# Performance work log

Hardware: AMD Instinct MI355X
Metric: run time of the kernel (lower is better)

The kernel has to match this reference:

```python
import jax, jax.numpy as jnp
import numpy as np

N_NODES = 20000
N_EDGES = 600000
HID = 128
HEADS = 4
NUM_IN = 2 * HID
N_BATCH = 64


def _gelu(x):
    return jax.nn.gelu(x, approximate=False)


def _bn(x, g, b, eps=1e-5):
    # BatchNorm1d, training-mode math: biased variance over the batch dim
    m = jnp.mean(x, axis=0)
    v = jnp.var(x, axis=0)
    return g * (x - m) * jax.lax.rsqrt(v + eps) + b


def setup_inputs() -> dict:
    keys = iter(jax.random.split(jax.random.key(0), 64))

    def nk():
        return next(keys)

    def lin(i, o):
        return (jax.random.normal(nk(), (i, o), jnp.float32) / np.sqrt(i)).astype(jnp.float32)

    def zeros(o):
        return jnp.zeros((o,), jnp.float32)

    inp = {
        "h_V": jax.random.normal(nk(), (N_NODES, HID), jnp.float32),
        "h_E": jax.random.normal(nk(), (N_EDGES, HID), jnp.float32),
        "edge_idx": jax.random.randint(nk(), (2, N_EDGES), 0, N_NODES),
        "batch_id": jnp.sort(jax.random.randint(nk(), (N_NODES,), 0, N_BATCH)),
        # NeighborAttention.W_V (num_in -> hid -> hid -> hid)
        "wv1_w": lin(NUM_IN, HID), "wv1_b": zeros(HID),
        "wv2_w": lin(HID, HID), "wv2_b": zeros(HID),
        "wv3_w": lin(HID, HID), "wv3_b": zeros(HID),
        # NeighborAttention.Bias (3*hid -> hid -> hid -> heads)
        "bb1_w": lin(3 * HID, HID), "bb1_b": zeros(HID),
        "bb2_w": lin(HID, HID), "bb2_b": zeros(HID),
        "bb3_w": lin(HID, HEADS), "bb3_b": zeros(HEADS),
        # NeighborAttention.W_O (no bias)
        "wo_w": lin(HID, HID),
        # GeneralGNN norms 0 and 1
        "n0_g": jnp.ones((HID,), jnp.float32), "n0_b": zeros(HID),
        "n1_g": jnp.ones((HID,), jnp.float32), "n1_b": zeros(HID),
        # dense FFN (hid -> 4*hid -> hid)
        "d1_w": lin(HID, 4 * HID), "d1_b": zeros(4 * HID),
        "d2_w": lin(4 * HID, HID), "d2_b": zeros(HID),
        # EdgeMLP (3*hid -> hid -> hid -> hid) + its norm
        "e1_w": lin(3 * HID, HID), "e1_b": zeros(HID),
        "e2_w": lin(HID, HID), "e2_b": zeros(HID),
        "e3_w": lin(HID, HID), "e3_b": zeros(HID),
        "en_g": jnp.ones((HID,), jnp.float32), "en_b": zeros(HID),
    }
    return inp


def _forward(h_V, h_E, src, dst,
             wv1_w, wv1_b, wv2_w, wv2_b, wv3_w, wv3_b,
             bb1_w, bb1_b, bb2_w, bb2_b, bb3_w, bb3_b,
             wo_w, n0_g, n0_b, n1_g, n1_b,
             d1_w, d1_b, d2_w, d2_b,
             e1_w, e1_b, e2_w, e2_b, e3_w, e3_b, en_g, en_b):
    N = h_V.shape[0]
    d_head = HID // HEADS
    # attention input: cat([h_E, h_V[dst]]) with center_id = src
    h_E_in = jnp.concatenate([h_E, h_V[dst]], axis=-1)  # (E, 2*HID)
    x = jnp.concatenate([h_V[src], h_E_in], axis=-1)     # (E, 3*HID)
    # Bias MLP -> per-edge per-head logits; the sqrt(d) * 1/sqrt(d) scaling cancels
    w = _gelu(x @ bb1_w + bb1_b)
    w = _gelu(w @ bb2_w + bb2_b)
    w = w @ bb3_w + bb3_b                                 # (E, HEADS)
    # value MLP
    V = _gelu(h_E_in @ wv1_w + wv1_b)
    V = _gelu(V @ wv2_w + wv2_b)
    V = (V @ wv3_w + wv3_b).reshape(-1, HEADS, d_head)    # (E, HEADS, d)
    # scatter_softmax over edges sharing a source node
    m = jax.ops.segment_max(w, src, num_segments=N)
    m = jnp.where(jnp.isfinite(m), m, 0.0)
    ew = jnp.exp(w - m[src])
    denom = jax.ops.segment_sum(ew, src, num_segments=N)
    attend = ew / denom[src]                              # (E, HEADS)
    agg = jax.ops.segment_sum(attend[:, :, None] * V, src, num_segments=N)
    dh = agg.reshape(N, HID) @ wo_w                       # W_O
    h_V = _bn(h_V + dh, n0_g, n0_b)
    dh = _gelu(h_V @ d1_w + d1_b) @ d2_w + d2_b           # dense FFN
    h_V = _bn(h_V + dh, n1_g, n1_b)
    # EdgeMLP update
    h_EV = jnp.concatenate([h_V[src], h_E, h_V[dst]], axis=-1)
    msg = _gelu(h_EV @ e1_w + e1_b)
    msg = _gelu(msg @ e2_w + e2_b)
    msg = msg @ e3_w + e3_b
    h_E = _bn(h_E + msg, en_g, en_b)
    # Context with node_context=edge_context=0 is identity
    return (h_V, h_E)


def reference(h_V, h_E, edge_idx, batch_id,
              wv1_w, wv1_b, wv2_w, wv2_b, wv3_w, wv3_b,
              bb1_w, bb1_b, bb2_w, bb2_b, bb3_w, bb3_b,
              wo_w, n0_g, n0_b, n1_g, n1_b,
              d1_w, d1_b, d2_w, d2_b,
              e1_w, e1_b, e2_w, e2_b, e3_w, e3_b, en_g, en_b):
    src, dst = edge_idx[0], edge_idx[1]
    return _forward(h_V, h_E, src, dst,
                    wv1_w, wv1_b, wv2_w, wv2_b, wv3_w, wv3_b,
                    bb1_w, bb1_b, bb2_w, bb2_b, bb3_w, bb3_b,
                    wo_w, n0_g, n0_b, n1_g, n1_b,
                    d1_w, d1_b, d2_w, d2_b,
                    e1_w, e1_b, e2_w, e2_b, e3_w, e3_b, en_g, en_b)
```

## Files before the change

### kernel.cpp

```cpp
#include <hip/hip_runtime.h>
#include <cstdint>
#include <cstddef>

#define NN 20000
#define NE 600000

typedef unsigned short u16;
typedef unsigned int   u32;
typedef __bf16 bf16x8 __attribute__((ext_vector_type(8)));
typedef float  f32x4  __attribute__((ext_vector_type(4)));

constexpr int PK_BB1 = 0;
constexpr int PK_BB2 = PK_BB1 + 384 * 128;
constexpr int PK_WV1 = PK_BB2 + 128 * 128;
constexpr int PK_WV2 = PK_WV1 + 256 * 128;
constexpr int PK_WV3 = PK_WV2 + 128 * 128;
constexpr int PK_WO  = PK_WV3 + 128 * 128;
constexpr int PK_D1  = PK_WO  + 128 * 128;
constexpr int PK_D2  = PK_D1  + 128 * 512;
constexpr int PK_E1  = PK_D2  + 512 * 128;
constexpr int PK_E2  = PK_E1  + 384 * 128;
constexpr int PK_E3  = PK_E2  + 128 * 128;
constexpr int PK_BB3 = PK_E3  + 128 * 128;

constexpr size_t WS_PW    = 0;
constexpr size_t WS_STATS = 0x100000;
constexpr size_t WS_FLAG  = WS_STATS + 3072;
constexpr size_t WS_HIST  = WS_STATS + 0x1000;
constexpr size_t WS_OFFS  = WS_HIST + 0x14000;
constexpr size_t WS_CNT   = WS_OFFS + 0x14000;
constexpr size_t WS_EIDS  = WS_CNT + 0x14000;
constexpr size_t WS_WLOG  = WS_EIDS + 0x250000;
constexpr size_t WS_AGG   = WS_WLOG + 0x930000;
constexpr size_t WS_R     = WS_AGG + 0xA00000;

__device__ __forceinline__ float bf2f(u16 u) {
    return __builtin_bit_cast(float, (u32)u << 16);
}
__device__ __forceinline__ u16 f2bf(float f) {
    return __builtin_bit_cast(u16, static_cast<__bf16>(f));
}
__device__ __forceinline__ float gelu_f(float x) {
    float z = fabsf(x) * 0.70710678118654752f;
    float t = __builtin_amdgcn_rcpf(fmaf(0.3275911f, z, 1.0f));
    float p = t * fmaf(t, fmaf(t, fmaf(t, fmaf(t, 1.061405429f, -1.453152027f),
                                       1.421413741f), -0.284496736f), 0.254829592f);
    float erfz = fmaf(-p, __expf(-z * z), 1.0f);
    float u = 0.5f * x;
    return fmaf(copysignf(erfz, x), u, u);
}
__device__ __forceinline__ float ldv(const void* p, size_t i, int m) {
    return m ? ((const float*)p)[i] : bf2f(((const u16*)p)[i]);
}
#define MFMA(a, b, c) __builtin_amdgcn_mfma_f32_16x16x32_bf16(a, b, c, 0, 0, 0)

#define TM 32
#define XS 136

__device__ __forceinline__ void mma128(const u16* __restrict__ xl, const u16* __restrict__ wp,
                                       int kcBase, int nDiv16, int wave, int lane,
                                       f32x4 acc[2][2]) {
#pragma unroll
    for (int kc = 0; kc < 4; ++kc) {
        int koff = kc * 32 + (lane >> 4) * 8;
        bf16x8 a0 = *(const bf16x8*)&xl[((lane & 15)) * XS + koff];
        bf16x8 a1 = *(const bf16x8*)&xl[((lane & 15) + 16) * XS + koff];
#pragma unroll
        for (int ni = 0; ni < 2; ++ni) {
            int nc = wave * 2 + ni;
            bf16x8 b = *(const bf16x8*)&wp[(((size_t)(kcBase + kc) * nDiv16 + nc) * 64 + lane) * 8];
            acc[0][ni] = MFMA(a0, b, acc[0][ni]);
            acc[1][ni] = MFMA(a1, b, acc[1][ni]);
        }
    }
}

__device__ __forceinline__ void epi_lds(f32x4 acc[2][2], u16* hl, const void* biasG,
                                        int wave, int lane, bool doGelu, int f32m) {
    int col0 = wave * 32;
#pragma unroll
    for (int ni = 0; ni < 2; ++ni) {
        int col = col0 + ni * 16 + (lane & 15);
        float b = ldv(biasG, col, f32m);
#pragma unroll
        for (int mi = 0; mi < 2; ++mi) {
            int rb = mi * 16 + (lane >> 4) * 4;
#pragma unroll
            for (int r = 0; r < 4; ++r) {
                float v = acc[mi][ni][r] + b;
                if (doGelu) v = gelu_f(v);
                hl[(rb + r) * XS + col] = f2bf(v);
            }
        }
    }
}

__device__ __forceinline__ void stage_row8(u16* dst8, const void* table, size_t row, int c8, int f32m) {
    if (f32m) {
        const float* s = (const float*)table + row * 128 + c8 * 8;
        float4 v0 = *(const float4*)s;
        float4 v1 = *(const float4*)(s + 4);
        uint4 o;
        o.x = (u32)f2bf(v0.x) | ((u32)f2bf(v0.y) << 16);
        o.y = (u32)f2bf(v0.z) | ((u32)f2bf(v0.w) << 16);
        o.z = (u32)f2bf(v1.x) | ((u32)f2bf(v1.y) << 16);
        o.w = (u32)f2bf(v1.z) | ((u32)f2bf(v1.w) << 16);
        *(uint4*)dst8 = o;
    } else {
        *(uint4*)dst8 = *(const uint4*)((const u16*)table + row * 128 + c8 * 8);
    }
}

__device__ __forceinline__ void stage_gidx(u16* dst, const void* table, const int* gIdx,
                                           int tid, int f32m) {
    int r0 = tid >> 4, c = tid & 15;
#pragma unroll
    for (int p = 0; p < 2; ++p) {
        int r = r0 + p * 16;
        stage_row8(&dst[r * XS + c * 8], table, (size_t)gIdx[r], c, f32m);
    }
}
__device__ __forceinline__ void stage_seq(u16* dst, const void* table, size_t rowBase, int tid, int f32m) {
    int r0 = tid >> 4, c = tid & 15;
#pragma unroll
    for (int p = 0; p < 2; ++p) {
        int r = r0 + p * 16;
        stage_row8(&dst[r * XS + c * 8], table, rowBase + r, c, f32m);
    }
}

__global__ void k_detect(const void* hV, int* flag) {
    int l = threadIdx.x;
    const u16* p = (const u16*)hV;
    float m = fmaxf(fabsf(bf2f(p[l])), fabsf(bf2f(p[64 + l])));
    for (int s = 1; s < 64; s <<= 1) m = fmaxf(m, __shfl_xor(m, s));
    if (l == 0) *flag = (m > 1e4f) ? 1 : 0;
}

__global__ void k_pack(const void* bb1, const void* bb2, const void* wv1, const void* wv2,
                       const void* wv3, const void* wo, const void* d1, const void* d2,
                       const void* e1, const void* e2, const void* e3, const void* bb3,
                       u16* pw, const int* dflag) {
    int f32m = *dflag;
    const int Ks[12] = {384, 128, 256, 128, 128, 128, 128, 512, 384, 128, 128, 128};
    const int Ns[12] = {128, 128, 128, 128, 128, 128, 512, 128, 128, 128, 128, 16};
    const void* srcs[12] = {bb1, bb2, wv1, wv2, wv3, wo, d1, d2, e1, e2, e3, bb3};
    int gid = blockIdx.x * 256 + threadIdx.x;
    int lane = gid & 63;
    int fid = gid >> 6;
    if (fid >= 708) return;
    int w = 0, base = 0, dstoff = 0;
    for (int i = 0; i < 12; ++i) {
        int nf = (Ks[i] / 32) * (Ns[i] / 16);
        if (fid < base + nf) { w = i; break; }
        base += nf;
        dstoff += Ks[i] * Ns[i];
    }
    int f = fid - base;
    int N = Ns[w];
    int kc = f / (N / 16), nc = f % (N / 16);
    const void* S = srcs[w];
    u16* D = pw + dstoff + ((size_t)f * 64 + lane) * 8;
    int krow = kc * 32 + (lane >> 4) * 8;
    int col = nc * 16 + (lane & 15);
#pragma unroll
    for (int j = 0; j < 8; ++j) {
        float v;
        if (w == 11) v = (col < 4) ? ldv(S, (size_t)(krow + j) * 4 + col, f32m) : 0.f;
        else         v = ldv(S, (size_t)(krow + j) * N + col, f32m);
        D[j] = f2bf(v);
    }
}

__global__ void k_hist(const int* src, int* hist) {
    int e = blockIdx.x * 256 + threadIdx.x;
    if (e < NE) atomicAdd(&hist[src[e]], 1);
}

__global__ void k_scan(const int* hist, int* offs, int* cnt) {
    __shared__ int buf[1024];
    __shared__ int carry;
    if (threadIdx.x == 0) carry = 0;
    __syncthreads();
    for (int b = 0; b < NN; b += 1024) {
        int i = b + threadIdx.x;
        int v = (i < NN) ? hist[i] : 0;
        buf[threadIdx.x] = v;
        __syncthreads();
        for (int s = 1; s < 1024; s <<= 1) {
            int t = (threadIdx.x >= s) ? buf[threadIdx.x - s] : 0;
            __syncthreads();
            buf[threadIdx.x] += t;
            __syncthreads();
        }
        int excl = buf[threadIdx.x] - v + carry;
        if (i < NN) { offs[i] = excl; cnt[i] = excl; }
        __syncthreads();
        if (threadIdx.x == 1023) carry += buf[1023];
        __syncthreads();
    }
    if (threadIdx.x == 0) offs[NN] = carry;
}

__global__ void k_fill(const int* src, int* cnt, int* eids) {
    int e = blockIdx.x * 256 + threadIdx.x;
    if (e < NE) {
        int slot = atomicAdd(&cnt[src[e]], 1);
        eids[slot] = e;
    }
}

__global__ __launch_bounds__(256, 2) void k_edge1(
    const void* __restrict__ hV, const void* __restrict__ hE, const int* __restrict__ eidx,
    const u16* __restrict__ pw, const void* bb1b, const void* bb2b,
    const void* bb3b, const void* wv1b, const void* wv2b, const void* wv3b,
    float* __restrict__ wlog, void* __restrict__ dout, const int* dflag) {
    __shared__ __attribute__((aligned(16))) u16 X[TM * XS];
    __shared__ __attribute__((aligned(16))) u16 Y[TM * XS];
    __shared__ __attribute__((aligned(16))) u16 Z[TM * XS];
    int f32m = *dflag;
    int tid = threadIdx.x, wave = tid >> 6, lane = tid & 63;
    long e0 = (long)blockIdx.x * TM;

    stage_gidx(X, hV, eidx + e0, tid, f32m);
    stage_seq (Y, hE, (size_t)e0, tid, f32m);
    stage_gidx(Z, hV, eidx + NE + e0, tid, f32m);
    __syncthreads();
    f32x4 accB[2][2] = {};
    f32x4 accV[2][2] = {};
    mma128(X, pw + PK_BB1, 0, 8, wave, lane, accB);
    mma128(Y, pw + PK_BB1, 4, 8, wave, lane, accB);
    mma128(Z, pw + PK_BB1, 8, 8, wave, lane, accB);
    mma128(Y, pw + PK_WV1, 0, 8, wave, lane, accV);
    mma128(Z, pw + PK_WV1, 4, 8, wave, lane, accV);
    __syncthreads();
    epi_lds(accB, X, bb1b, wave, lane, true, f32m);
    epi_lds(accV, Y, wv1b, wave, lane, true, f32m);
    __syncthreads();
    f32x4 accB2[2][2] = {};
    f32x4 accV2[2][2] = {};
    mma128(X, pw + PK_BB2, 0, 8, wave, lane, accB2);
    mma128(Y, pw + PK_WV2, 0, 8, wave, lane, accV2);
    __syncthreads();
    epi_lds(accB2, Z, bb2b, wave, lane, true, f32m);
    epi_lds(accV2, X, wv2b, wave, lane, true, f32m);
    __syncthreads();
    u16* Vout = (u16*)((char*)dout + (size_t)NN * 128 * (f32m ? 4 : 2));
    f32x4 accV3[2][2] = {};
    mma128(X, pw + PK_WV3, 0, 8, wave, lane, accV3);
    {
        int col0 = wave * 32;
#pragma unroll
        for (int ni = 0; ni < 2; ++ni) {
            int col = col0 + ni * 16 + (lane & 15);
            float b = ldv(wv3b, col, f32m);
#pragma unroll
            for (int mi = 0; mi < 2; ++mi) {
                int rb = mi * 16 + (lane >> 4) * 4;
#pragma unroll
                for (int r = 0; r < 4; ++r) {
                    long row = e0 + rb + r;
                    Vout[row * 128 + col] = f2bf(accV3[mi][ni][r] + b);
                }
            }
        }
    }
    if (wave == 0) {
        f32x4 aw0 = {0.f, 0.f, 0.f, 0.f};
        f32x4 aw1 = {0.f, 0.f, 0.f, 0.f};
#pragma unroll
        for (int kc = 0; kc < 4; ++kc) {
            int koff = kc * 32 + (lane >> 4) * 8;
            bf16x8 a0 = *(const bf16x8*)&Z[(lane & 15) * XS + koff];
            bf16x8 a1 = *(const bf16x8*)&Z[((lane & 15) + 16) * XS + koff];
            bf16x8 b = *(const bf16x8*)&pw[PK_BB3 + ((size_t)kc * 64 + lane) * 8];
            aw0 = MFMA(a0, b, aw0);
            aw1 = MFMA(a1, b, aw1);
        }
        if ((lane & 15) < 4) {
            int col = lane & 15;
            int rbase = (lane >> 4) * 4;
            float b3 = ldv(bb3b, col, f32m);
#pragma unroll
            for (int r = 0; r < 4; ++r) {
                wlog[(e0 + rbase + r) * 4 + col] = aw0[r] + b3;
                wlog[(e0 + 16 + rbase + r) * 4 + col] = aw1[r] + b3;
            }
        }
    }
}

__global__ void k_agg(const int* __restrict__ offs, const int* __restrict__ eids,
                      const float* __restrict__ wlog, const void* __restrict__ dout,
                      float* __restrict__ agg, const int* dflag) {
    int f32m = *dflag;
    const u16* V = (const u16*)((const char*)dout + (size_t)NN * 128 * (f32m ? 4 : 2));
    int node = blockIdx.x;
    int l = threadIdx.x;
    int beg = offs[node], end = offs[node + 1];
    int deg = end - beg;
    if (deg == 0) {
        agg[(size_t)node * 128 + 2 * l] = 0.f;
        agg[(size_t)node * 128 + 2 * l + 1] = 0.f;
        return;
    }
    int h = l & 3;
    float lmax = -3.0e38f;
    for (int i = (l >> 2); i < deg; i += 16) {
        int e = eids[beg + i];
        lmax = fmaxf(lmax, wlog[(size_t)e * 4 + h]);
    }
    for (int s = 4; s < 64; s <<= 1) lmax = fmaxf(lmax, __shfl_xor(lmax, s));
    float lsum = 0.f;
    for (int i = (l >> 2); i < deg; i += 16) {
        int e = eids[beg + i];
        lsum += __expf(wlog[(size_t)e * 4 + h] - lmax);
    }
    for (int s = 4; s < 64; s <<= 1) lsum += __shfl_xor(lsum, s);
    int hh = l >> 4;
    float mh = __shfl(lmax, hh);
    float inv = __builtin_amdgcn_rcpf(__shfl(lsum, hh));
    float a0 = 0.f, a1 = 0.f;
    for (int i = 0; i < deg; ++i) {
        int e = eids[beg + i];
        float aw = __expf(wlog[(size_t)e * 4 + hh] - mh) * inv;
        u32 vv = *(const u32*)&V[(size_t)e * 128 + 2 * l];
        a0 += aw * bf2f((u16)(vv & 0xffffu));
        a1 += aw * bf2f((u16)(vv >> 16));
    }
    float2 o;
    o.x = a0;
    o.y = a1;
    *(float2*)&agg[(size_t)node * 128 + 2 * l] = o;
}

__global__ __launch_bounds__(256, 2) void k_wo(const float* __restrict__ agg,
                                               const void* __restrict__ hV,
                                               const u16* __restrict__ pw,
                                               float* __restrict__ rbuf,
                                               float* __restrict__ stats0, const int* dflag) {
    __shared__ __attribute__((aligned(16))) u16 xb[TM * XS];
    __shared__ float lsum[128], lsq[128];
    int f32m = *dflag;
    int tid = threadIdx.x, wave = tid >> 6, lane = tid & 63;
    long n0 = (long)blockIdx.x * TM;
    if (tid < 128) { lsum[tid] = 0.f; lsq[tid] = 0.f; }
    {
        int r = tid >> 3, cc = (tid & 7) * 16;
        long row = n0 + r;
        for (int j = 0; j < 16; j += 4) {
            float4 v = {0.f, 0.f, 0.f, 0.f};
            if (row < NN) v = *(const float4*)&agg[row * 128 + cc + j];
            u16* d = &xb[r * XS + cc + j];
            d[0] = f2bf(v.x); d[1] = f2bf(v.y); d[2] = f2bf(v.z); d[3] = f2bf(v.w);
        }
    }
    __syncthreads();
    f32x4 acc[2][2] = {};
    mma128(xb, pw + PK_WO, 0, 8, wave, lane, acc);
    int col0 = wave * 32;
#pragma unroll
    for (int ni = 0; ni < 2; ++ni) {
        int col = col0 + ni * 16 + (lane & 15);
#pragma unroll
        for (int mi = 0; mi < 2; ++mi) {
            int rb = mi * 16 + (lane >> 4) * 4;
#pragma unroll
            for (int r = 0; r < 4; ++r) {
                long row = n0 + rb + r;
                if (row < NN) {
                    float v = ldv(hV, (size_t)row * 128 + col, f32m) + acc[mi][ni][r];
                    rbuf[row * 128 + col] = v;
                    atomicAdd(&lsum[col], v);
                    atomicAdd(&lsq[col], v * v);
                }
            }
        }
    }
    __syncthreads();
    if (tid < 128) {
        atomicAdd(&stats0[tid], lsum[tid]);
        atomicAdd(&stats0[128 + tid], lsq[tid]);
    }
}

__global__ __launch_bounds__(256, 2) void k_ffn(float* __restrict__ rbuf,
                                                const float* __restrict__ stats0,
                                                const void* n0g, const void* n0b,
                                                const u16* __restrict__ pw,
                                                const void* d1b, const void* d2b,
                                                float* __restrict__ stats1, const int* dflag) {
    __shared__ float bnS[128], bnB[128];
    __shared__ float h1f[TM * 128];
    __shared__ __attribute__((aligned(16))) u16 h1x[TM * XS];
    __shared__ __attribute__((aligned(16))) u16 hid[TM * 520];
    __shared__ float lsum[128], lsq[128];
    int f32m = *dflag;
    int tid = threadIdx.x, wave = tid >> 6, lane = tid & 63;
    long n0 = (long)blockIdx.x * TM;
    if (tid < 128) {
        float m = stats0[tid] * (1.f / NN);
        float v = stats0[128 + tid] * (1.f / NN) - m * m;
        float s = ldv(n0g, tid, f32m) * rsqrtf(v + 1e-5f);
        bnS[tid] = s;
        bnB[tid] = ldv(n0b, tid, f32m) - m * s;
        lsum[tid] = 0.f;
        lsq[tid] = 0.f;
    }
    __syncthreads();
    {
        int r = tid >> 3, cc = (tid & 7) * 16;
        long row = n0 + r;
        for (int j = 0; j < 16; ++j) {
            int c = cc + j;
            float v = (row < NN) ? (rbuf[row * 128 + c] * bnS[c] + bnB[c]) : 0.f;
            h1f[r * 128 + c] = v;
            h1x[r * XS + c] = f2bf(v);
        }
    }
    __syncthreads();
    f32x4 acc1[2][8] = {};
#pragma unroll
    for (int kc = 0; kc < 4; ++kc) {
        int koff = kc * 32 + (lane >> 4) * 8;
        bf16x8 a0 = *(const bf16x8*)&h1x[(lane & 15) * XS + koff];
        bf16x8 a1 = *(const bf16x8*)&h1x[((lane & 15) + 16) * XS + koff];
#pragma unroll
        for (int ni = 0; ni < 8; ++ni) {
            int nc = wave * 8 + ni;
            bf16x8 b = *(const bf16x8*)&pw[PK_D1 + (((size_t)kc * 32 + nc) * 64 + lane) * 8];
            acc1[0][ni] = MFMA(a0, b, acc1[0][ni]);
            acc1[1][ni] = MFMA(a1, b, acc1[1][ni]);
        }
    }
#pragma unroll
    for (int ni = 0; ni < 8; ++ni) {
        int col = wave * 128 + ni * 16 + (lane & 15);
        float bb = ldv(d1b, col, f32m);
#pragma unroll
        for (int mi = 0; mi < 2; ++mi) {
            int rb = mi * 16 + (lane >> 4) * 4;
#pragma unroll
            for (int r = 0; r < 4; ++r)
                hid[(rb + r) * 520 + col] = f2bf(gelu_f(acc1[mi][ni][r] + bb));
        }
    }
    __syncthreads();
    f32x4 acc2[2][2] = {};
#pragma unroll
    for (int kc = 0; kc < 16; ++kc) {
        int koff = kc * 32 + (lane >> 4) * 8;
        bf16x8 a0 = *(const bf16x8*)&hid[(lane & 15) * 520 + koff];
        bf16x8 a1 = *(const bf16x8*)&hid[((lane & 15) + 16) * 520 + koff];
#pragma unroll
        for (int ni = 0; ni < 2; ++ni) {
            int nc = wave * 2 + ni;
            bf16x8 b = *(const bf16x8*)&pw[PK_D2 + (((size_t)kc * 8 + nc) * 64 + lane) * 8];
            acc2[0][ni] = MFMA(a0, b, acc2[0][ni]);
            acc2[1][ni] = MFMA(a1, b, acc2[1][ni]);
        }
    }
    int col0 = wave * 32;
#pragma unroll
    for (int ni = 0; ni < 2; ++ni) {
        int col = col0 + ni * 16 + (lane & 15);
        float db = ldv(d2b, col, f32m);
#pragma unroll
        for (int mi = 0; mi < 2; ++mi) {
            int rb = mi * 16 + (lane >> 4) * 4;
#pragma unroll
            for (int r = 0; r < 4; ++r) {
                long row = n0 + rb + r;
                if (row < NN) {
                    float v = h1f[(rb + r) * 128 + col] + acc2[mi][ni][r] + db;
                    rbuf[row * 128 + col] = v;
                    atomicAdd(&lsum[col], v);
                    atomicAdd(&lsq[col], v * v);
                }
            }
        }
    }
    __syncthreads();
    if (tid < 128) {
        atomicAdd(&stats1[tid], lsum[tid]);
        atomicAdd(&stats1[128 + tid], lsq[tid]);
    }
}

__global__ void k_out_hV(const float* __restrict__ rbuf, const float* __restrict__ stats1,
                         const void* n1g, const void* n1b, void* __restrict__ dout,
                         const int* dflag) {
    int f32m = *dflag;
    int idx = blockIdx.x * 256 + threadIdx.x;
    if (idx >= NN * 128) return;
    int c = idx & 127;
    float m = stats1[c] * (1.f / NN);
    float v = stats1[128 + c] * (1.f / NN) - m * m;
    float s = ldv(n1g, c, f32m) * rsqrtf(v + 1e-5f);
    float b = ldv(n1b, c, f32m) - m * s;
    float o = rbuf[idx] * s + b;
    if (f32m) ((float*)dout)[idx] = o;
    else      ((u16*)dout)[idx] = f2bf(o);
}

__global__ __launch_bounds__(256, 2) void k_edge2(
    const void* __restrict__ hE, const int* __restrict__ eidx,
    const u16* __restrict__ pw, const void* e1b, const void* e2b, const void* e3b,
    void* __restrict__ dout, float* __restrict__ statsE, const int* dflag) {
    __shared__ __attribute__((aligned(16))) u16 X[TM * XS];
    __shared__ __attribute__((aligned(16))) u16 Y[TM * XS];
    __shared__ __attribute__((aligned(16))) u16 Z[TM * XS];
    int f32m = *dflag;
    int tid = threadIdx.x, wave = tid >> 6, lane = tid & 63;
    long e0 = (long)blockIdx.x * TM;
    const void* hV2 = dout;

    stage_gidx(X, hV2, eidx + e0, tid, f32m);
    stage_seq (Z, hE, (size_t)e0, tid, f32m);
    stage_gidx(Y, hV2, eidx + NE + e0, tid, f32m);
    int col0 = wave * 32, rbase = (lane >> 4) * 4, cl = lane & 15;
    float res[2][2][4];
#pragma unroll
    for (int ni = 0; ni < 2; ++ni)
#pragma unroll
        for (int mi = 0; mi < 2; ++mi)
#pragma unroll
            for (int r = 0; r < 4; ++r)
                res[ni][mi][r] = ldv(hE, (size_t)(e0 + mi * 16 + rbase + r) * 128
                                              + col0 + ni * 16 + cl, f32m);
    __syncthreads();
    f32x4 a1[2][2] = {};
    mma128(X, pw + PK_E1, 0, 8, wave, lane, a1);
    mma128(Z, pw + PK_E1, 4, 8, wave, lane, a1);
    mma128(Y, pw + PK_E1, 8, 8, wave, lane, a1);
    __syncthreads();
    epi_lds(a1, X, e1b, wave, lane, true, f32m);
    __syncthreads();
    f32x4 a2[2][2] = {};
    mma128(X, pw + PK_E2, 0, 8, wave, lane, a2);
    epi_lds(a2, Y, e2b, wave, lane, true, f32m);
    __syncthreads();
    f32x4 a3[2][2] = {};
    mma128(Y, pw + PK_E3, 0, 8, wave, lane, a3);
    float* yb32 = (float*)((char*)dout + (size_t)NN * 512);
    u16*   yb16 = (u16*)((char*)dout + (size_t)NN * 256);
    float ssum[2] = {0.f, 0.f}, ssq[2] = {0.f, 0.f};
#pragma unroll
    for (int ni = 0; ni < 2; ++ni) {
        int col = col0 + ni * 16 + cl;
        float b = ldv(e3b, col, f32m);
#pragma unroll
        for (int mi = 0; mi < 2; ++mi) {
            int rb = mi * 16 + rbase;
#pragma unroll
            for (int r = 0; r < 4; ++r) {
                long row = e0 + rb + r;
                float y = res[ni][mi][r] + a3[mi][ni][r] + b;
                if (f32m) yb32[row * 128 + col] = y;
                else      yb16[row * 128 + col] = f2bf(y);
                ssum[ni] += y;
                ssq[ni] += y * y;
            }
        }
    }
#pragma unroll
    for (int ni = 0; ni < 2; ++ni) {
        ssum[ni] += __shfl_xor(ssum[ni], 16);
        ssum[ni] += __shfl_xor(ssum[ni], 32);
        ssq[ni]  += __shfl_xor(ssq[ni], 16);
        ssq[ni]  += __shfl_xor(ssq[ni], 32);
    }
    if (lane < 16) {
#pragma unroll
        for (int ni = 0; ni < 2; ++ni) {
            int col = col0 + ni * 16 + lane;
            atomicAdd(&statsE[col], ssum[ni]);
            atomicAdd(&statsE[128 + col], ssq[ni]);
        }
    }
}

__global__ void k_out_hE(const float* __restrict__ statsE, const void* eng, const void* enb,
                         void* __restrict__ dout, const int* dflag) {
    int f32m = *dflag;
    long i4 = (long)blockIdx.x * 256 + threadIdx.x;
    if (i4 >= (long)NE * 32) return;
    int c0 = (int)((i4 & 31) * 4);
    float s[4], b[4];
#pragma unroll
    for (int j = 0; j < 4; ++j) {
        int c = c0 + j;
        float m = statsE[c] * (1.f / NE);
        float v = statsE[128 + c] * (1.f / NE) - m * m;
        float sc = ldv(eng, c, f32m) * rsqrtf(v + 1e-5f);
        s[j] = sc;
        b[j] = ldv(enb, c, f32m) - m * sc;
    }
    if (f32m) {
        float4* y = (float4*)((char*)dout + (size_t)NN * 512);
        float4 v = y[i4];
        v.x = v.x * s[0] + b[0];
        v.y = v.y * s[1] + b[1];
        v.z = v.z * s[2] + b[2];
        v.w = v.w * s[3] + b[3];
        y[i4] = v;
    } else {
        ushort4* y = (ushort4*)((char*)dout + (size_t)NN * 256);
        ushort4 v = y[i4];
        v.x = f2bf(bf2f(v.x) * s[0] + b[0]);
        v.y = f2bf(bf2f(v.y) * s[1] + b[1]);
        v.z = f2bf(bf2f(v.z) * s[2] + b[2]);
        v.w = f2bf(bf2f(v.w) * s[3] + b[3]);
        y[i4] = v;
    }
}

extern "C" void kernel_launch(void* const* d_in, const int* in_sizes, int n_in,
                              void* d_out, int out_size, void* d_ws, size_t ws_size,
                              hipStream_t stream) {
    (void)in_sizes; (void)n_in; (void)out_size; (void)ws_size;
    const void* hV = d_in[0];
    const void* hE = d_in[1];
    const int* eidx = (const int*)d_in[2];
    const void* wv1w = d_in[4];  const void* wv1b = d_in[5];
    const void* wv2w = d_in[6];  const void* wv2b = d_in[7];
    const void* wv3w = d_in[8];  const void* wv3b = d_in[9];
    const void* bb1w = d_in[10]; const void* bb1b = d_in[11];
    const void* bb2w = d_in[12]; const void* bb2b = d_in[13];
    const void* bb3w = d_in[14]; const void* bb3b = d_in[15];
    const void* wow  = d_in[16];
    const void* n0g = d_in[17]; const void* n0b = d_in[18];
    const void* n1g = d_in[19]; const void* n1b = d_in[20];
    const void* d1w = d_in[21]; const void* d1b = d_in[22];
    const void* d2w = d_in[23]; const void* d2b = d_in[24];
    const void* e1w = d_in[25]; const void* e1b = d_in[26];
    const void* e2w = d_in[27]; const void* e2b = d_in[28];
    const void* e3w = d_in[29]; const void* e3b = d_in[30];
    const void* eng = d_in[31]; const void* enb = d_in[32];

    char* ws = (char*)d_ws;
    u16* pw      = (u16*)(ws + WS_PW);
    float* stats = (float*)(ws + WS_STATS);
    int* dflag   = (int*)(ws + WS_FLAG);
    int* hist    = (int*)(ws + WS_HIST);
    int* offs    = (int*)(ws + WS_OFFS);
    int* cnt     = (int*)(ws + WS_CNT);
    int* eids    = (int*)(ws + WS_EIDS);
    float* wlog  = (float*)(ws + WS_WLOG);
    float* agg   = (float*)(ws + WS_AGG);
    float* rbuf  = (float*)(ws + WS_R);

    hipMemsetAsync(ws + WS_STATS, 0, 0x1000 + NN * sizeof(int), stream);

    k_detect<<<1, 64, 0, stream>>>(hV, dflag);
    k_pack<<<177, 256, 0, stream>>>(bb1w, bb2w, wv1w, wv2w, wv3w, wow, d1w, d2w,
                                    e1w, e2w, e3w, bb3w, pw, dflag);
    k_hist<<<(NE + 255) / 256, 256, 0, stream>>>(eidx, hist);
    k_scan<<<1, 1024, 0, stream>>>(hist, offs, cnt);
    k_fill<<<(NE + 255) / 256, 256, 0, stream>>>(eidx, cnt, eids);
    k_edge1<<<NE / TM, 256, 0, stream>>>(hV, hE, eidx, pw, bb1b, bb2b, bb3b,
                                         wv1b, wv2b, wv3b, wlog, d_out, dflag);
    k_agg<<<NN, 64, 0, stream>>>(offs, eids, wlog, d_out, agg, dflag);
    k_wo<<<(NN + TM - 1) / TM, 256, 0, stream>>>(agg, hV, pw, rbuf, stats, dflag);
    k_ffn<<<(NN + TM - 1) / TM, 256, 0, stream>>>(rbuf, stats, n0g, n0b, pw, d1b, d2b,
                                                  stats + 256, dflag);
    k_out_hV<<<(NN * 128 + 255) / 256, 256, 0, stream>>>(rbuf, stats + 256, n1g, n1b, d_out, dflag);
    k_edge2<<<NE / TM, 256, 0, stream>>>(hE, eidx, pw, e1b, e2b, e3b, d_out, stats + 512, dflag);
    k_out_hE<<<(int)(((long)NE * 32 + 255) / 256), 256, 0, stream>>>(stats + 512, eng, enb, d_out, dflag);
}
```

Measured before the change: 1.905 ms.

## Precompute per-node first-layer projections and gather them per edge

The first linear layer of the edge bias, value and EdgeMLP paths is split by input block. The node-dependent parts (h_V[src]·W, h_V[dst]·W) are computed once per node in new k_pre1/k_pre2 kernels and gathered per edge as fp32 partial sums, so each edge kernel only runs the h_E block of the matmul. This removes roughly two thirds of the first-layer MFMA work per edge. In exchange it adds fp32 gather traffic, two times 128 floats per edge per path instead of bf16 rows, and reuses the agg/rbuf workspace and spare output space as scratch.

Result: no change. 1.886 ms (-1.0%).

```diff
diff --git a/kernel.cpp b/kernel.cpp
--- a/kernel.cpp
+++ b/kernel.cpp
@@ -33,6 +33,7 @@
 constexpr size_t WS_WLOG  = WS_EIDS + 0x250000;
 constexpr size_t WS_AGG   = WS_WLOG + 0x930000;
 constexpr size_t WS_R     = WS_AGG + 0xA00000;
+constexpr size_t WS_PV    = WS_R + 0xA00000;
 
 __device__ __forceinline__ float bf2f(u16 u) {
     return __builtin_bit_cast(float, (u32)u << 16);
@@ -91,6 +92,23 @@
                 if (doGelu) v = gelu_f(v);
                 hl[(rb + r) * XS + col] = f2bf(v);
             }
+        }
+    }
+}
+
+__device__ __forceinline__ void epi_gadd(f32x4 acc[2][2], const float g[2][2][4], u16* hl,
+                                         const void* biasG, int wave, int lane, int f32m) {
+    int col0 = wave * 32;
+#pragma unroll
+    for (int ni = 0; ni < 2; ++ni) {
+        int col = col0 + ni * 16 + (lane & 15);
+        float b = ldv(biasG, col, f32m);
+#pragma unroll
+        for (int mi = 0; mi < 2; ++mi) {
+            int rb = mi * 16 + (lane >> 4) * 4;
+#pragma unroll
+            for (int r = 0; r < 4; ++r)
+                hl[(rb + r) * XS + col] = f2bf(gelu_f(acc[mi][ni][r] + g[mi][ni][r] + b));
         }
     }
 }
@@ -111,15 +129,6 @@
     }
 }
 
-__device__ __forceinline__ void stage_gidx(u16* dst, const void* table, const int* gIdx,
-                                           int tid, int f32m) {
-    int r0 = tid >> 4, c = tid & 15;
-#pragma unroll
-    for (int p = 0; p < 2; ++p) {
-        int r = r0 + p * 16;
-        stage_row8(&dst[r * XS + c * 8], table, (size_t)gIdx[r], c, f32m);
-    }
-}
 __device__ __forceinline__ void stage_seq(u16* dst, const void* table, size_t rowBase, int tid, int f32m) {
     int r0 = tid >> 4, c = tid & 15;
 #pragma unroll
@@ -210,53 +219,125 @@
     }
 }
 
+__global__ __launch_bounds__(256, 2) void k_pre1(
+    const void* __restrict__ hV, const u16* __restrict__ pw,
+    float* __restrict__ pa, float* __restrict__ pc,
+    void* __restrict__ dout, float* __restrict__ pvws, const int* dflag) {
+    __shared__ __attribute__((aligned(16))) u16 xb[TM * XS];
+    int f32m = *dflag;
+    float* pv = f32m ? (float*)((char*)dout + (size_t)NN * 512 + (size_t)NE * 256) : pvws;
+    int tid = threadIdx.x, wave = tid >> 6, lane = tid & 63;
+    long n0 = (long)blockIdx.x * TM;
+    stage_seq(xb, hV, (size_t)n0, tid, f32m);
+    __syncthreads();
+    f32x4 aA[2][2] = {}, aC[2][2] = {}, aV[2][2] = {};
+    mma128(xb, pw + PK_BB1, 0, 8, wave, lane, aA);
+    mma128(xb, pw + PK_BB1, 8, 8, wave, lane, aC);
+    mma128(xb, pw + PK_WV1, 4, 8, wave, lane, aV);
+    int col0 = wave * 32, rbase = (lane >> 4) * 4, cl = lane & 15;
+#pragma unroll
+    for (int ni = 0; ni < 2; ++ni) {
+        int col = col0 + ni * 16 + cl;
+#pragma unroll
+        for (int mi = 0; mi < 2; ++mi)
+#pragma unroll
+            for (int r = 0; r < 4; ++r) {
+                size_t row = (size_t)(n0 + mi * 16 + rbase + r);
+                pa[row * 128 + col] = aA[mi][ni][r];
+                pc[row * 128 + col] = aC[mi][ni][r];
+                pv[row * 128 + col] = aV[mi][ni][r];
+            }
+    }
+}
+
+__global__ __launch_bounds__(256, 2) void k_pre2(
+    const void* __restrict__ hV2, const u16* __restrict__ pw,
+    float* __restrict__ p2a, float* __restrict__ p2c, const int* dflag) {
+    __shared__ __attribute__((aligned(16))) u16 xb[TM * XS];
+    int f32m = *dflag;
+    int tid = threadIdx.x, wave = tid >> 6, lane = tid & 63;
+    long n0 = (long)blockIdx.x * TM;
+    stage_seq(xb, hV2, (size_t)n0, tid, f32m);
+    __syncthreads();
+    f32x4 aA[2][2] = {}, aC[2][2] = {};
+    mma128(xb, pw + PK_E1, 0, 8, wave, lane, aA);
+    mma128(xb, pw + PK_E1, 8, 8, wave, lane, aC);
+    int col0 = wave * 32, rbase = (lane >> 4) * 4, cl = lane & 15;
+#pragma unroll
+    for (int ni = 0; ni < 2; ++ni) {
+        int col = col0 + ni * 16 + cl;
+#pragma unroll
+        for (int mi = 0; mi < 2; ++mi)
+#pragma unroll
+            for (int r = 0; r < 4; ++r) {
+                size_t row = (size_t)(n0 + mi * 16 + rbase + r);
+                p2a[row * 128 + col] = aA[mi][ni][r];
+                p2c[row * 128 + col] = aC[mi][ni][r];
+            }
+    }
+}
+
 __global__ __launch_bounds__(256, 2) void k_edge1(
-    const void* __restrict__ hV, const void* __restrict__ hE, const int* __restrict__ eidx,
-    const u16* __restrict__ pw, const void* bb1b, const void* bb2b,
-    const void* bb3b, const void* wv1b, const void* wv2b, const void* wv3b,
-    float* __restrict__ wlog, void* __restrict__ dout, const int* dflag) {
+    const void* __restrict__ hE, const int* __restrict__ eidx,
+    const u16* __restrict__ pw,
+    const float* __restrict__ pa, const float* __restrict__ pc,
+    const void* bb1b, const void* bb2b, const void* bb3b,
+    const void* wv1b, const void* wv2b, const void* wv3b,
+    float* __restrict__ wlog, void* __restrict__ dout,
+    const float* __restrict__ pvws, const int* dflag) {
     __shared__ __attribute__((aligned(16))) u16 X[TM * XS];
     __shared__ __attribute__((aligned(16))) u16 Y[TM * XS];
     __shared__ __attribute__((aligned(16))) u16 Z[TM * XS];
     int f32m = *dflag;
+    const float* pv = f32m ? (const float*)((const char*)dout + (size_t)NN * 512 + (size_t)NE * 256)
+                           : pvws;
     int tid = threadIdx.x, wave = tid >> 6, lane = tid & 63;
     long e0 = (long)blockIdx.x * TM;
 
-    stage_gidx(X, hV, eidx + e0, tid, f32m);
-    stage_seq (Y, hE, (size_t)e0, tid, f32m);
-    stage_gidx(Z, hV, eidx + NE + e0, tid, f32m);
+    stage_seq(Y, hE, (size_t)e0, tid, f32m);
+    int col0 = wave * 32, rbase = (lane >> 4) * 4, cl = lane & 15;
+    float gB[2][2][4], gV[2][2][4];
+#pragma unroll
+    for (int mi = 0; mi < 2; ++mi)
+#pragma unroll
+        for (int r = 0; r < 4; ++r) {
+            long row = e0 + mi * 16 + rbase + r;
+            size_t s = (size_t)eidx[row];
+            size_t d = (size_t)eidx[NE + row];
+#pragma unroll
+            for (int ni = 0; ni < 2; ++ni) {
+                int col = col0 + ni * 16 + cl;
+                gB[mi][ni][r] = pa[s * 128 + col] + pc[d * 128 + col];
+                gV[mi][ni][r] = pv[d * 128 + col];
+            }
+        }
     __syncthreads();
     f32x4 accB[2][2] = {};
     f32x4 accV[2][2] = {};
-    mma128(X, pw + PK_BB1, 0, 8, wave, lane, accB);
     mma128(Y, pw + PK_BB1, 4, 8, wave, lane, accB);
-    mma128(Z, pw + PK_BB1, 8, 8, wave, lane, accB);
     mma128(Y, pw + PK_WV1, 0, 8, wave, lane, accV);
-    mma128(Z, pw + PK_WV1, 4, 8, wave, lane, accV);
-    __syncthreads();
-    epi_lds(accB, X, bb1b, wave, lane, true, f32m);
-    epi_lds(accV, Y, wv1b, wave, lane, true, f32m);
+    epi_gadd(accB, gB, X, bb1b, wave, lane, f32m);
+    epi_gadd(accV, gV, Z, wv1b, wave, lane, f32m);
     __syncthreads();
     f32x4 accB2[2][2] = {};
     f32x4 accV2[2][2] = {};
     mma128(X, pw + PK_BB2, 0, 8, wave, lane, accB2);
-    mma128(Y, pw + PK_WV2, 0, 8, wave, lane, accV2);
-    __syncthreads();
-    epi_lds(accB2, Z, bb2b, wave, lane, true, f32m);
+    mma128(Z, pw + PK_WV2, 0, 8, wave, lane, accV2);
+    epi_lds(accB2, Y, bb2b, wave, lane, true, f32m);
+    __syncthreads();
     epi_lds(accV2, X, wv2b, wave, lane, true, f32m);
     __syncthreads();
     u16* Vout = (u16*)((char*)dout + (size_t)NN * 128 * (f32m ? 4 : 2));
     f32x4 accV3[2][2] = {};
     mma128(X, pw + PK_WV3, 0, 8, wave, lane, accV3);
     {
-        int col0 = wave * 32;
 #pragma unroll
         for (int ni = 0; ni < 2; ++ni) {
-            int col = col0 + ni * 16 + (lane & 15);
+            int col = col0 + ni * 16 + cl;
             float b = ldv(wv3b, col, f32m);
 #pragma unroll
             for (int mi = 0; mi < 2; ++mi) {
-                int rb = mi * 16 + (lane >> 4) * 4;
+                int rb = mi * 16 + rbase;
 #pragma unroll
                 for (int r = 0; r < 4; ++r) {
                     long row = e0 + rb + r;
@@ -271,15 +352,14 @@
 #pragma unroll
         for (int kc = 0; kc < 4; ++kc) {
             int koff = kc * 32 + (lane >> 4) * 8;
-            bf16x8 a0 = *(const bf16x8*)&Z[(lane & 15) * XS + koff];
-            bf16x8 a1 = *(const bf16x8*)&Z[((lane & 15) + 16) * XS + koff];
+            bf16x8 a0 = *(const bf16x8*)&Y[(lane & 15) * XS + koff];
+            bf16x8 a1 = *(const bf16x8*)&Y[((lane & 15) + 16) * XS + koff];
             bf16x8 b = *(const bf16x8*)&pw[PK_BB3 + ((size_t)kc * 64 + lane) * 8];
             aw0 = MFMA(a0, b, aw0);
             aw1 = MFMA(a1, b, aw1);
         }
         if ((lane & 15) < 4) {
             int col = lane & 15;
-            int rbase = (lane >> 4) * 4;
             float b3 = ldv(bb3b, col, f32m);
 #pragma unroll
             for (int r = 0; r < 4; ++r) {
@@ -505,43 +585,44 @@
 
 __global__ __launch_bounds__(256, 2) void k_edge2(
     const void* __restrict__ hE, const int* __restrict__ eidx,
-    const u16* __restrict__ pw, const void* e1b, const void* e2b, const void* e3b,
+    const u16* __restrict__ pw,
+    const float* __restrict__ p2a, const float* __restrict__ p2c,
+    const void* e1b, const void* e2b, const void* e3b,
     void* __restrict__ dout, float* __restrict__ statsE, const int* dflag) {
     __shared__ __attribute__((aligned(16))) u16 X[TM * XS];
     __shared__ __attribute__((aligned(16))) u16 Y[TM * XS];
-    __shared__ __attribute__((aligned(16))) u16 Z[TM * XS];
     int f32m = *dflag;
     int tid = threadIdx.x, wave = tid >> 6, lane = tid & 63;
     long e0 = (long)blockIdx.x * TM;
-    const void* hV2 = dout;
-
-    stage_gidx(X, hV2, eidx + e0, tid, f32m);
-    stage_seq (Z, hE, (size_t)e0, tid, f32m);
-    stage_gidx(Y, hV2, eidx + NE + e0, tid, f32m);
+
+    stage_seq(X, hE, (size_t)e0, tid, f32m);
     int col0 = wave * 32, rbase = (lane >> 4) * 4, cl = lane & 15;
-    float res[2][2][4];
-#pragma unroll
-    for (int ni = 0; ni < 2; ++ni)
-#pragma unroll
-        for (int mi = 0; mi < 2; ++mi)
-#pragma unroll
-            for (int r = 0; r < 4; ++r)
-                res[ni][mi][r] = ldv(hE, (size_t)(e0 + mi * 16 + rbase + r) * 128
-                                              + col0 + ni * 16 + cl, f32m);
+    float g1[2][2][4], res[2][2][4];
+#pragma unroll
+    for (int mi = 0; mi < 2; ++mi)
+#pragma unroll
+        for (int r = 0; r < 4; ++r) {
+            long row = e0 + mi * 16 + rbase + r;
+            size_t s = (size_t)eidx[row];
+            size_t d = (size_t)eidx[NE + row];
+#pragma unroll
+            for (int ni = 0; ni < 2; ++ni) {
+                int col = col0 + ni * 16 + cl;
+                g1[mi][ni][r] = p2a[s * 128 + col] + p2c[d * 128 + col];
+                res[mi][ni][r] = ldv(hE, (size_t)row * 128 + col, f32m);
+            }
+        }
     __syncthreads();
     f32x4 a1[2][2] = {};
-    mma128(X, pw + PK_E1, 0, 8, wave, lane, a1);
-    mma128(Z, pw + PK_E1, 4, 8, wave, lane, a1);
-    mma128(Y, pw + PK_E1, 8, 8, wave, lane, a1);
-    __syncthreads();
-    epi_lds(a1, X, e1b, wave, lane, true, f32m);
+    mma128(X, pw + PK_E1, 4, 8, wave, lane, a1);
+    epi_gadd(a1, g1, Y, e1b, wave, lane, f32m);
     __syncthreads();
     f32x4 a2[2][2] = {};
-    mma128(X, pw + PK_E2, 0, 8, wave, lane, a2);
-    epi_lds(a2, Y, e2b, wave, lane, true, f32m);
+    mma128(Y, pw + PK_E2, 0, 8, wave, lane, a2);
+    epi_lds(a2, X, e2b, wave, lane, true, f32m);
     __syncthreads();
     f32x4 a3[2][2] = {};
-    mma128(Y, pw + PK_E3, 0, 8, wave, lane, a3);
+    mma128(X, pw + PK_E3, 0, 8, wave, lane, a3);
     float* yb32 = (float*)((char*)dout + (size_t)NN * 512);
     u16*   yb16 = (u16*)((char*)dout + (size_t)NN * 256);
     float ssum[2] = {0.f, 0.f}, ssq[2] = {0.f, 0.f};
@@ -555,7 +636,7 @@
 #pragma unroll
             for (int r = 0; r < 4; ++r) {
                 long row = e0 + rb + r;
-                float y = res[ni][mi][r] + a3[mi][ni][r] + b;
+                float y = res[mi][ni][r] + a3[mi][ni][r] + b;
                 if (f32m) yb32[row * 128 + col] = y;
                 else      yb16[row * 128 + col] = f2bf(y);
                 ssum[ni] += y;
@@ -649,6 +730,7 @@
     float* wlog  = (float*)(ws + WS_WLOG);
     float* agg   = (float*)(ws + WS_AGG);
     float* rbuf  = (float*)(ws + WS_R);
+    float* pvws  = (float*)(ws + WS_PV);
 
     hipMemsetAsync(ws + WS_STATS, 0, 0x1000 + NN * sizeof(int), stream);
 
@@ -658,13 +740,16 @@
     k_hist<<<(NE + 255) / 256, 256, 0, stream>>>(eidx, hist);
     k_scan<<<1, 1024, 0, stream>>>(hist, offs, cnt);
     k_fill<<<(NE + 255) / 256, 256, 0, stream>>>(eidx, cnt, eids);
-    k_edge1<<<NE / TM, 256, 0, stream>>>(hV, hE, eidx, pw, bb1b, bb2b, bb3b,
-                                         wv1b, wv2b, wv3b, wlog, d_out, dflag);
+    k_pre1<<<NN / TM, 256, 0, stream>>>(hV, pw, agg, rbuf, d_out, pvws, dflag);
+    k_edge1<<<NE / TM, 256, 0, stream>>>(hE, eidx, pw, agg, rbuf, bb1b, bb2b, bb3b,
+                                         wv1b, wv2b, wv3b, wlog, d_out, pvws, dflag);
     k_agg<<<NN, 64, 0, stream>>>(offs, eids, wlog, d_out, agg, dflag);
     k_wo<<<(NN + TM - 1) / TM, 256, 0, stream>>>(agg, hV, pw, rbuf, stats, dflag);
     k_ffn<<<(NN + TM - 1) / TM, 256, 0, stream>>>(rbuf, stats, n0g, n0b, pw, d1b, d2b,
                                                   stats + 256, dflag);
     k_out_hV<<<(NN * 128 + 255) / 256, 256, 0, stream>>>(rbuf, stats + 256, n1g, n1b, d_out, dflag);
-    k_edge2<<<NE / TM, 256, 0, stream>>>(hE, eidx, pw, e1b, e2b, e3b, d_out, stats + 512, dflag);
+    k_pre2<<<NN / TM, 256, 0, stream>>>(d_out, pw, agg, rbuf, dflag);
+    k_edge2<<<NE / TM, 256, 0, stream>>>(hE, eidx, pw, agg, rbuf, e1b, e2b, e3b,
+                                         d_out, stats + 512, dflag);
     k_out_hE<<<(int)(((long)NE * 32 + 255) / 256), 256, 0, stream>>>(stats + 512, eng, enb, d_out, dflag);
 }
```
